# Kernel tuning notes

Hardware: AMD Instinct MI355X
Metric: run time of the kernel (lower is better)

Reference implementation:

```python
import jax, jax.numpy as jnp
import numpy as np

N_NODES = 50000
N_PAIRS = 1_600_000
D_IN = 128
D_OUT = 128


def setup_inputs() -> dict:
    key = jax.random.key(0)
    k1, k2, k3, k4, k5, k6 = jax.random.split(key, 6)
    features = jax.random.normal(k1, (N_NODES, D_IN), dtype=jnp.float32)
    pair_w = jax.random.uniform(k2, (N_PAIRS,), dtype=jnp.float32)  # cosine weights per pair
    # Xavier-uniform init for the projection weight, zeros for bias (as in torch module)
    limit = float(np.sqrt(6.0 / (D_IN + D_OUT)))
    weight = jax.random.uniform(k3, (D_IN, D_OUT), dtype=jnp.float32, minval=-limit, maxval=limit)
    bias = jnp.zeros((D_OUT,), dtype=jnp.float32)
    pair_i = jax.random.randint(k4, (N_PAIRS,), 0, N_NODES)
    pair_j = jax.random.randint(k5, (N_PAIRS,), 0, N_NODES)
    node_idx = jnp.sort(jax.random.randint(k6, (N_PAIRS,), 0, N_NODES))  # center node per pair
    return {"features": features, "pair_w": pair_w, "weight": weight, "bias": bias,
            "pair_i": pair_i, "pair_j": pair_j, "node_idx": node_idx}


def reference(features, pair_w, weight, bias, pair_i, pair_j, node_idx):
    # Per pair: (features[i] + features[j]) * cos_weight  -> [n_pairs, d_in]
    msgs = (features[pair_i] + features[pair_j]) * pair_w[:, None]
    # Accumulate into the center node of each pair -> [n_nodes, d_in]
    agg = jax.ops.segment_sum(msgs, node_idx, num_segments=N_NODES)
    # Final linear projection
    return agg @ weight + bias
```

## Files before the change

kernel.cpp:

```cpp
#include <hip/hip_runtime.h>

#define D 128

typedef __attribute__((ext_vector_type(8))) short short8;
typedef __attribute__((ext_vector_type(4))) float floatx4;

__device__ __forceinline__ float bf_lo(unsigned u) { return __uint_as_float(u << 16); }
__device__ __forceinline__ float bf_hi(unsigned u) { return __uint_as_float(u & 0xffff0000u); }
__device__ __forceinline__ unsigned pack_bf16(float a, float b) {
    unsigned ua = __float_as_uint(a), ub = __float_as_uint(b);
    ua = (ua + 0x7fffu + ((ua >> 16) & 1u)) >> 16;
    ub = (ub + 0x7fffu + ((ub >> 16) & 1u)) >> 16;
    return ua | (ub << 16);
}

__global__ __launch_bounds__(256) void prep_kernel(
    const float* __restrict__ F, const float* __restrict__ pw,
    const float* __restrict__ W, const int* __restrict__ pi,
    const int* __restrict__ pj, const int* __restrict__ nidx,
    unsigned* __restrict__ Fb, unsigned long long* __restrict__ rec,
    int* __restrict__ offs, unsigned* __restrict__ Wt,
    int n_nodes, int n_pairs) {
    const int B1 = (n_nodes * (D / 4) + 255) / 256;
    const int B2 = (n_pairs + 255) / 256;
    const int b = blockIdx.x;
    if (b < B1) {
        int t = b * 256 + threadIdx.x;
        if (t >= n_nodes * (D / 4)) return;
        float4 v = reinterpret_cast<const float4*>(F)[t];
        uint2 o = {pack_bf16(v.x, v.y), pack_bf16(v.z, v.w)};
        reinterpret_cast<uint2*>(Fb)[t] = o;
    } else if (b < B1 + B2) {
        int p = (b - B1) * 256 + threadIdx.x;
        if (p >= n_pairs) return;
        unsigned ijv = (unsigned)pi[p] | ((unsigned)pj[p] << 16);
        rec[p] = (unsigned long long)ijv |
                 ((unsigned long long)__float_as_uint(pw[p]) << 32);
        int cur  = nidx[p];
        int prev = p ? nidx[p - 1] : -1;
        for (int n = prev + 1; n <= cur; ++n) offs[n] = p;
        if (p == n_pairs - 1)
            for (int n = cur + 1; n <= n_nodes; ++n) offs[n] = n_pairs;
    } else {
        int t = (b - B1 - B2) * 256 + threadIdx.x;
        if (t >= D * (D / 2)) return;
        int c = t >> 6, kk = t & 63;
        Wt[t] = pack_bf16(W[(2 * kk) * D + c], W[(2 * kk + 1) * D + c]);
    }
}

#define PAIR_BODY(r)                                                          \
    {                                                                         \
        const unsigned ij_ = (unsigned)(r);                                   \
        const unsigned i_  = ij_ & 0xffffu;                                   \
        const unsigned j_  = ij_ >> 16;                                       \
        const float    w_  = __uint_as_float((unsigned)((r) >> 32));          \
        const uint4 ui = *reinterpret_cast<const uint4*>(base + (size_t)i_ * 64); \
        const uint4 uj = *reinterpret_cast<const uint4*>(base + (size_t)j_ * 64); \
        a0 += (bf_lo(ui.x) + bf_lo(uj.x)) * w_;                               \
        a1 += (bf_hi(ui.x) + bf_hi(uj.x)) * w_;                               \
        a2 += (bf_lo(ui.y) + bf_lo(uj.y)) * w_;                               \
        a3 += (bf_hi(ui.y) + bf_hi(uj.y)) * w_;                               \
        a4 += (bf_lo(ui.z) + bf_lo(uj.z)) * w_;                               \
        a5 += (bf_hi(ui.z) + bf_hi(uj.z)) * w_;                               \
        a6 += (bf_lo(ui.w) + bf_lo(uj.w)) * w_;                               \
        a7 += (bf_hi(ui.w) + bf_hi(uj.w)) * w_;                               \
    }

__global__ __launch_bounds__(256) void aggregate_kernel(
    const unsigned* __restrict__ Fb, const unsigned long long* __restrict__ rec,
    const int* __restrict__ offs, unsigned* __restrict__ aggb, int n_nodes) {
    const int cg  = blockIdx.x & 1;
    const int wid = threadIdx.x >> 6;
    const int n   = (blockIdx.x >> 1) * 4 + wid;
    if (n >= n_nodes) return;
    const int start = offs[n];
    const int end   = offs[n + 1];
    const int lane  = threadIdx.x & 7;
    const int g     = (threadIdx.x >> 3) & 7;

    const unsigned* __restrict__ base = Fb + cg * 32 + lane * 4;

    float a0 = 0.f, a1 = 0.f, a2 = 0.f, a3 = 0.f;
    float a4 = 0.f, a5 = 0.f, a6 = 0.f, a7 = 0.f;

    int p = start;
    for (; p + 32 <= end; p += 32) {
        unsigned long long r0 = __builtin_nontemporal_load(rec + p + 0 * 8 + g);
        unsigned long long r1 = __builtin_nontemporal_load(rec + p + 1 * 8 + g);
        unsigned long long r2 = __builtin_nontemporal_load(rec + p + 2 * 8 + g);
        unsigned long long r3 = __builtin_nontemporal_load(rec + p + 3 * 8 + g);
        PAIR_BODY(r0)
        PAIR_BODY(r1)
        PAIR_BODY(r2)
        PAIR_BODY(r3)
    }
    if (p + 16 <= end) {
        unsigned long long r0 = __builtin_nontemporal_load(rec + p + 0 * 8 + g);
        unsigned long long r1 = __builtin_nontemporal_load(rec + p + 1 * 8 + g);
        PAIR_BODY(r0)
        PAIR_BODY(r1)
        p += 16;
    }
    for (int q = p + g; q < end; q += 8) {
        unsigned long long r = __builtin_nontemporal_load(rec + q);
        PAIR_BODY(r)
    }

#pragma unroll
    for (int m = 8; m <= 32; m <<= 1) {
        a0 += __shfl_xor(a0, m); a1 += __shfl_xor(a1, m);
        a2 += __shfl_xor(a2, m); a3 += __shfl_xor(a3, m);
        a4 += __shfl_xor(a4, m); a5 += __shfl_xor(a5, m);
        a6 += __shfl_xor(a6, m); a7 += __shfl_xor(a7, m);
    }

    if (g == 0) {
        uint4 o = {pack_bf16(a0, a1), pack_bf16(a2, a3),
                   pack_bf16(a4, a5), pack_bf16(a6, a7)};
        *reinterpret_cast<uint4*>(aggb + (size_t)n * 64 + cg * 32 + lane * 4) = o;
    }
}

__global__ __launch_bounds__(256) void proj_kernel(
    const unsigned* __restrict__ aggb, const unsigned* __restrict__ Wt,
    const float* __restrict__ bias, float* __restrict__ out, int M) {
    const int wid = threadIdx.x >> 6;
    const int l   = threadIdx.x & 63;
    const int lr  = l & 15;
    const int lk  = l >> 4;
    const int row_base = blockIdx.x * 64 + wid * 16;

    int arow = row_base + lr;
    if (arow >= M) arow = M - 1;

    const short8* __restrict__ A8 = reinterpret_cast<const short8*>(aggb);
    const short8* __restrict__ B8 = reinterpret_cast<const short8*>(Wt);

    floatx4 acc[8];
#pragma unroll
    for (int t = 0; t < 8; ++t) acc[t] = (floatx4){0.f, 0.f, 0.f, 0.f};

#pragma unroll
    for (int ks = 0; ks < 4; ++ks) {
        const short8 a = A8[(size_t)arow * 16 + ks * 4 + lk];
#pragma unroll
        for (int t = 0; t < 8; ++t) {
            const short8 bfr = B8[(size_t)(t * 16 + lr) * 16 + ks * 4 + lk];
            acc[t] = __builtin_amdgcn_mfma_f32_16x16x32_bf16(a, bfr, acc[t], 0, 0, 0);
        }
    }

#pragma unroll
    for (int t = 0; t < 8; ++t) {
        const float bcol = bias[t * 16 + lr];
#pragma unroll
        for (int r = 0; r < 4; ++r) {
            const int row = row_base + lk * 4 + r;
            if (row < M)
                out[(size_t)row * D + t * 16 + lr] = acc[t][r] + bcol;
        }
    }
}

extern "C" void kernel_launch(void* const* d_in, const int* in_sizes, int n_in,
                              void* d_out, int out_size, void* d_ws, size_t ws_size,
                              hipStream_t stream) {
    const float* F    = (const float*)d_in[0];
    const float* pw   = (const float*)d_in[1];
    const float* W    = (const float*)d_in[2];
    const float* bias = (const float*)d_in[3];
    const int*   pi   = (const int*)d_in[4];
    const int*   pj   = (const int*)d_in[5];
    const int*   nidx = (const int*)d_in[6];
    float* out = (float*)d_out;

    const int n_pairs = in_sizes[1];
    const int n_nodes = in_sizes[0] / D;

    const size_t aggb_bytes = (size_t)n_nodes * D * 2;
    const size_t offs_bytes = ((size_t)(n_nodes + 1) * 4 + 255) & ~(size_t)255;
    const size_t rec_bytes  = (size_t)n_pairs * 8;
    const size_t wt_bytes   = (size_t)D * (D / 2) * 4;
    const size_t fb_bytes   = (size_t)n_nodes * D * 2;

    char* pp = (char*)d_ws;
    unsigned* aggb = (unsigned*)pp;                pp += aggb_bytes;
    int*      offs = (int*)pp;                     pp += offs_bytes;
    unsigned long long* rec = (unsigned long long*)pp;  pp += rec_bytes;
    unsigned* Wt   = (unsigned*)pp;                pp += wt_bytes;
    size_t used = (size_t)(pp - (char*)d_ws);
    unsigned* Fb = (ws_size >= used + fb_bytes)
                 ? (unsigned*)pp
                 : (unsigned*)d_out;

    const int B1 = (n_nodes * (D / 4) + 255) / 256;
    const int B2 = (n_pairs + 255) / 256;
    const int B3 = (D * (D / 2) + 255) / 256;
    prep_kernel<<<B1 + B2 + B3, 256, 0, stream>>>(F, pw, W, pi, pj, nidx,
                                                  Fb, rec, offs, Wt,
                                                  n_nodes, n_pairs);
    const int nb = (n_nodes + 3) / 4;
    aggregate_kernel<<<nb * 2, 256, 0, stream>>>(Fb, rec, offs, aggb, n_nodes);
    proj_kernel<<<(n_nodes + 63) / 64, 256, 0, stream>>>(aggb, Wt, bias, out, n_nodes);
}
```

Baseline: 117.6 us.

## Split bf16 feature table into four column-group planes for cache-resident gathers

Feature rows are stored as four separate 32-column planes, and the aggregation kernel launches four column groups per node block, with 16 pair-groups of 4 lanes each per wavefront. Each plane is smaller, so the random row gathers for one column group are more likely to stay resident in cache. In exchange, the pair records are read four times instead of twice, and the unrolled multi-record inner loop is replaced by a simple strided loop with less memory-level parallelism per thread.

```diff
diff --git a/kernel.cpp b/kernel.cpp
--- a/kernel.cpp
+++ b/kernel.cpp
@@ -1,6 +1,7 @@
 #include <hip/hip_runtime.h>
 
 #define D 128
+#define NCG 4
 
 typedef __attribute__((ext_vector_type(8))) short short8;
 typedef __attribute__((ext_vector_type(4))) float floatx4;
@@ -27,9 +28,11 @@
     if (b < B1) {
         int t = b * 256 + threadIdx.x;
         if (t >= n_nodes * (D / 4)) return;
+        int n = t >> 5, q = t & 31;
         float4 v = reinterpret_cast<const float4*>(F)[t];
         uint2 o = {pack_bf16(v.x, v.y), pack_bf16(v.z, v.w)};
-        reinterpret_cast<uint2*>(Fb)[t] = o;
+        int cg = q >> 3, qq = q & 7;
+        reinterpret_cast<uint2*>(Fb + (size_t)(cg * n_nodes + n) * 16)[qq] = o;
     } else if (b < B1 + B2) {
         int p = (b - B1) * 256 + threadIdx.x;
         if (p >= n_pairs) return;
@@ -49,66 +52,43 @@
     }
 }
 
-#define PAIR_BODY(r)                                                          \
-    {                                                                         \
-        const unsigned ij_ = (unsigned)(r);                                   \
-        const unsigned i_  = ij_ & 0xffffu;                                   \
-        const unsigned j_  = ij_ >> 16;                                       \
-        const float    w_  = __uint_as_float((unsigned)((r) >> 32));          \
-        const uint4 ui = *reinterpret_cast<const uint4*>(base + (size_t)i_ * 64); \
-        const uint4 uj = *reinterpret_cast<const uint4*>(base + (size_t)j_ * 64); \
-        a0 += (bf_lo(ui.x) + bf_lo(uj.x)) * w_;                               \
-        a1 += (bf_hi(ui.x) + bf_hi(uj.x)) * w_;                               \
-        a2 += (bf_lo(ui.y) + bf_lo(uj.y)) * w_;                               \
-        a3 += (bf_hi(ui.y) + bf_hi(uj.y)) * w_;                               \
-        a4 += (bf_lo(ui.z) + bf_lo(uj.z)) * w_;                               \
-        a5 += (bf_hi(ui.z) + bf_hi(uj.z)) * w_;                               \
-        a6 += (bf_lo(ui.w) + bf_lo(uj.w)) * w_;                               \
-        a7 += (bf_hi(ui.w) + bf_hi(uj.w)) * w_;                               \
-    }
-
 __global__ __launch_bounds__(256) void aggregate_kernel(
     const unsigned* __restrict__ Fb, const unsigned long long* __restrict__ rec,
     const int* __restrict__ offs, unsigned* __restrict__ aggb, int n_nodes) {
-    const int cg  = blockIdx.x & 1;
+    const int cg  = blockIdx.x & (NCG - 1);
     const int wid = threadIdx.x >> 6;
-    const int n   = (blockIdx.x >> 1) * 4 + wid;
+    const int n   = (blockIdx.x >> 2) * 4 + wid;
     if (n >= n_nodes) return;
     const int start = offs[n];
     const int end   = offs[n + 1];
-    const int lane  = threadIdx.x & 7;
-    const int g     = (threadIdx.x >> 3) & 7;
+    const int lane  = threadIdx.x & 3;
+    const int g     = (threadIdx.x >> 2) & 15;
 
-    const unsigned* __restrict__ base = Fb + cg * 32 + lane * 4;
+    const unsigned* __restrict__ base = Fb + (size_t)cg * n_nodes * 16 + lane * 4;
 
     float a0 = 0.f, a1 = 0.f, a2 = 0.f, a3 = 0.f;
     float a4 = 0.f, a5 = 0.f, a6 = 0.f, a7 = 0.f;
 
-    int p = start;
-    for (; p + 32 <= end; p += 32) {
-        unsigned long long r0 = __builtin_nontemporal_load(rec + p + 0 * 8 + g);
-        unsigned long long r1 = __builtin_nontemporal_load(rec + p + 1 * 8 + g);
-        unsigned long long r2 = __builtin_nontemporal_load(rec + p + 2 * 8 + g);
-        unsigned long long r3 = __builtin_nontemporal_load(rec + p + 3 * 8 + g);
-        PAIR_BODY(r0)
-        PAIR_BODY(r1)
-        PAIR_BODY(r2)
-        PAIR_BODY(r3)
-    }
-    if (p + 16 <= end) {
-        unsigned long long r0 = __builtin_nontemporal_load(rec + p + 0 * 8 + g);
-        unsigned long long r1 = __builtin_nontemporal_load(rec + p + 1 * 8 + g);
-        PAIR_BODY(r0)
-        PAIR_BODY(r1)
-        p += 16;
-    }
-    for (int q = p + g; q < end; q += 8) {
-        unsigned long long r = __builtin_nontemporal_load(rec + q);
-        PAIR_BODY(r)
+    for (int p = start + g; p < end; p += 16) {
+        const unsigned long long r = __builtin_nontemporal_load(rec + p);
+        const unsigned ij_ = (unsigned)r;
+        const unsigned i_  = ij_ & 0xffffu;
+        const unsigned j_  = ij_ >> 16;
+        const float    w_  = __uint_as_float((unsigned)(r >> 32));
+        const uint4 ui = *reinterpret_cast<const uint4*>(base + (size_t)i_ * 16);
+        const uint4 uj = *reinterpret_cast<const uint4*>(base + (size_t)j_ * 16);
+        a0 += (bf_lo(ui.x) + bf_lo(uj.x)) * w_;
+        a1 += (bf_hi(ui.x) + bf_hi(uj.x)) * w_;
+        a2 += (bf_lo(ui.y) + bf_lo(uj.y)) * w_;
+        a3 += (bf_hi(ui.y) + bf_hi(uj.y)) * w_;
+        a4 += (bf_lo(ui.z) + bf_lo(uj.z)) * w_;
+        a5 += (bf_hi(ui.z) + bf_hi(uj.z)) * w_;
+        a6 += (bf_lo(ui.w) + bf_lo(uj.w)) * w_;
+        a7 += (bf_hi(ui.w) + bf_hi(uj.w)) * w_;
     }
 
 #pragma unroll
-    for (int m = 8; m <= 32; m <<= 1) {
+    for (int m = 4; m <= 32; m <<= 1) {
         a0 += __shfl_xor(a0, m); a1 += __shfl_xor(a1, m);
         a2 += __shfl_xor(a2, m); a3 += __shfl_xor(a3, m);
         a4 += __shfl_xor(a4, m); a5 += __shfl_xor(a5, m);
@@ -118,7 +98,7 @@
     if (g == 0) {
         uint4 o = {pack_bf16(a0, a1), pack_bf16(a2, a3),
                    pack_bf16(a4, a5), pack_bf16(a6, a7)};
-        *reinterpret_cast<uint4*>(aggb + (size_t)n * 64 + cg * 32 + lane * 4) = o;
+        *reinterpret_cast<uint4*>(aggb + (size_t)n * 64 + cg * 16 + lane * 4) = o;
     }
 }
 
@@ -201,6 +181,6 @@
                                                   Fb, rec, offs, Wt,
                                                   n_nodes, n_pairs);
     const int nb = (n_nodes + 3) / 4;
-    aggregate_kernel<<<nb * 2, 256, 0, stream>>>(Fb, rec, offs, aggb, n_nodes);
+    aggregate_kernel<<<nb * NCG, 256, 0, stream>>>(Fb, rec, offs, aggb, n_nodes);
     proj_kernel<<<(n_nodes + 63) / 64, 256, 0, stream>>>(aggb, Wt, bias, out, n_nodes);
 }
```

New measurement: 153.7 us. +30.7%, slower.
